# Performance work log

Hardware: AMD Instinct MI355X
Metric: run time of the kernel (lower is better)

The kernel has to match this reference:

```python
import jax, jax.numpy as jnp
import numpy as np

K = 5          # top_k periods
KERNEL = 25    # moving-average kernel for series decomposition
D = 64         # d_model / channels
EPS = 1e-5     # BatchNorm eps (torch default)


def setup_inputs() -> dict:
    key = jax.random.key(0)
    k0, k1, k2, k3, k4 = jax.random.split(key, 5)
    B, T = 8, 2048
    x = jax.random.normal(k0, (B, T, D), jnp.float32)
    w1 = jax.random.normal(k1, (D, D, 3, 3), jnp.float32) * 0.05
    w2 = jax.random.normal(k2, (D, D, 3, 3), jnp.float32) * 0.05
    bn1_gamma = jnp.ones((D,), jnp.float32) + 0.1 * jax.random.normal(k3, (D,), jnp.float32)
    bn2_gamma = jnp.ones((D,), jnp.float32) + 0.1 * jax.random.normal(k4, (D,), jnp.float32)
    z = jnp.zeros((D,), jnp.float32)
    o = jnp.ones((D,), jnp.float32)
    return dict(x=x, w1=w1, w2=w2,
                bn1_gamma=bn1_gamma, bn1_beta=z, bn1_mean=z, bn1_var=o,
                bn2_gamma=bn2_gamma, bn2_beta=z, bn2_mean=z, bn2_var=o)


def _moving_avg(x, kernel):
    # AvgPool1d(stride=1, padding=(kernel-1)//2, count_include_pad=False) over time.
    T = x.shape[1]
    pad = (kernel - 1) // 2
    cs = jnp.concatenate([jnp.zeros_like(x[:, :1]), jnp.cumsum(x, axis=1)], axis=1)  # [B,T+1,C]
    t = jnp.arange(T)
    lo = jnp.clip(t - pad, 0, T)          # inclusive window start
    hi = jnp.clip(t + pad + 1, 0, T)      # exclusive window end
    sums = cs[:, hi] - cs[:, lo]
    return sums / (hi - lo).astype(x.dtype)[None, :, None]


def _auto_corr(s, k):
    T = s.shape[1]
    Xf = jnp.fft.rfft(s, axis=1)
    Pm = (Xf * jnp.conj(Xf)).real.mean(axis=-1)          # [B, T//2+1]
    r = jnp.fft.irfft(Pm, n=T, axis=1)                   # [B, T]
    r = r.at[:, 0].set(-jnp.inf)                          # forbid lag 0
    vals, idx = jax.lax.top_k(r, k)                       # [B,k]
    w = jax.nn.softmax(vals, axis=1)
    return idx, w


def _bn(z, gamma, beta, mean, var):
    return (z - mean) * (gamma * jax.lax.rsqrt(var + EPS)) + beta


def _process_one(s_b, p, w1, w2, bn1, bn2):
    # s_b: [T, C]; p: scalar int period.
    # Equivalent to: roll(s_b, -p), reflect-pad time to cyc*p, fold to [C,cyc,p],
    # Conv2dResBlock (3x3 zero-pad convs + eval BN + GELU + residual), unfold, crop to T.
    T, C = s_b.shape
    U = 2 * T - 2                               # static bound: cyc*p <= T+p-1 <= 2T-2
    u = jnp.arange(U)
    cyc = (T + p - 1) // p
    v = jnp.where(u < T, u, 2 * T - 2 - u)      # reflect extension index
    g = s_b[(v + p) % T]                         # [U,C] rolled-by-(-p) then reflect-padded
    r = u // p                                   # grid row (cycle)
    c = u % p                                    # grid col (phase)

    def conv3x3(z, w):
        # zero-padded 3x3 conv on the [cyc, p] grid, expressed on the flat time axis
        out = jnp.zeros_like(z)
        for dr in (-1, 0, 1):
            for dc in (-1, 0, 1):
                valid = (r + dr >= 0) & (r + dr < cyc) & (c + dc >= 0) & (c + dc < p)
                un = jnp.clip(u + dr * p + dc, 0, U - 1)
                zn = jnp.where(valid[:, None], z[un], 0.0)    # [U,C]
                out = out + zn @ w[:, :, dr + 1, dc + 1].T    # [U,Cout]
        return out

    h = _bn(conv3x3(g, w1), *bn1)
    h = jax.nn.gelu(h, approximate=False)
    h = _bn(conv3x3(h, w2), *bn2)
    return (g + h)[:T]                           # residual + unfold-crop


def reference(x, w1, w2, bn1_gamma, bn1_beta, bn1_mean, bn1_var,
              bn2_gamma, bn2_beta, bn2_mean, bn2_var):
    trend = _moving_avg(x, KERNEL)
    s = x - trend                                # seasonal
    idx, w = _auto_corr(s, K)                    # [B,K] periods, weights
    bn1 = (bn1_gamma, bn1_beta, bn1_mean, bn1_var)
    bn2 = (bn2_gamma, bn2_beta, bn2_mean, bn2_var)
    f = lambda sb, p: _process_one(sb, p, w1, w2, bn1, bn2)
    y = jax.vmap(lambda sb, pb: jax.vmap(lambda p: f(sb, p))(pb))(s, idx)  # [B,K,T,C]
    agg = jnp.einsum('bk,bktc->btc', w, y)
    return agg + trend + x
```

## Files before the change

kernel.cpp:

```cpp
#include <hip/hip_runtime.h>
#include <hip/hip_bf16.h>
#include <math.h>

#define TB 8
#define TT 2048
#define TD 64
#define TK 5
#define TPAD 12
#define EPSBN 1e-5f
#define UMAX 4096

#define ROWS 64
#define BAND 66
#define LROWS 198

#define ROWS2 16
#define BAND2 18
#define LROWS2 54
#define SH8   432
#define BUFB  6912

#define ACG 17

typedef __attribute__((ext_vector_type(8))) short short8;
typedef __attribute__((ext_vector_type(4))) float f32x4;

#define OFF_S     0
#define OFF_SBF   1048576
#define OFF_R     1572864
#define OFF_IDX   1581056
#define OFF_W     1581096
#define OFF_WT1   1581136
#define OFF_WT2   1599568
#define OFF_H1    1618000
#define OFF_CAND  6860880
#define OFF_VALS  6860944

__global__ __launch_bounds__(256) void k_trend(const float* __restrict__ x,
                                               float* __restrict__ out, float* __restrict__ s,
                                               __hip_bfloat16* __restrict__ sbf,
                                               const float* __restrict__ w1, const float* __restrict__ w2,
                                               __hip_bfloat16* __restrict__ wt1, __hip_bfloat16* __restrict__ wt2,
                                               float* __restrict__ r)
{
    if (blockIdx.x >= 256) {
        int d = (blockIdx.x - 256) * 256 + threadIdx.x;
        if (d < TB * 1024) r[d] = 0.f;
        if (d < 36864) {
            int j = d & 7, l = (d >> 3) & 63, nt = (d >> 9) & 3, kb = d >> 11;
            int tap = kb >> 1, half = kb & 1;
            int co = nt * 16 + (l & 15);
            int ci = half * 32 + (l >> 4) * 8 + j;
            int src = (co * 64 + ci) * 9 + tap;
            wt1[d] = __float2bfloat16(w1[src]);
            wt2[d] = __float2bfloat16(w2[src]);
        }
        return;
    }
    int gid = blockIdx.x * 256 + threadIdx.x;
    int c = gid & 63;
    int tblk = (gid >> 6) & 127;
    int b = gid >> 13;
    int t0 = tblk * 16;
    const float* base = x + (size_t)b * TT * TD + c;
    float sum = 0.f;
    for (int tt = t0 - TPAD; tt <= t0 + TPAD; ++tt)
        if (tt >= 0 && tt < TT) sum += base[(size_t)tt * TD];
    size_t o = (size_t)b * TT * TD + (size_t)t0 * TD + c;
    #pragma unroll
    for (int i = 0; i < 16; ++i) {
        int t = t0 + i;
        int lo = t - TPAD; if (lo < 0) lo = 0;
        int hi = t + TPAD; if (hi > TT - 1) hi = TT - 1;
        float tr = sum / (float)(hi - lo + 1);
        float xv = base[(size_t)t * TD];
        out[o] = xv + tr;
        float sv = xv - tr;
        s[o] = sv;
        sbf[o] = __float2bfloat16(sv);
        int addt = t + TPAD + 1, subt = t - TPAD;
        if (addt < TT) sum += base[(size_t)addt * TD];
        if (subt >= 0) sum -= base[(size_t)subt * TD];
        o += TD;
    }
}

__global__ __launch_bounds__(256) void k_ac_mfma(const short* __restrict__ sbf16, float* __restrict__ r)
{
    int id = blockIdx.x;
    int b = id & 7;
    int slot = id >> 3;
    int g = slot % ACG;
    int qq = slot / ACG;
    int d0 = g * 4;
    int t0 = qq * 32;
    const short* sb = sbf16 + (size_t)b * TT * TD;

    __shared__ short Atile[2][1024];
    __shared__ short Btile[6][1024];
    __shared__ float scr[4][16 * 17];

    int tid = threadIdx.x;
    if (tid < 128) {
        int dst = (tid * 16) ^ (((tid >> 3) & 7) << 4);
        *(short8*)((char*)Atile[t0 & 1] + dst) =
            *(const short8*)(sb + (size_t)((t0 & 127) * 1024) + tid * 8);
        #pragma unroll
        for (int j = 0; j < 4; ++j) {
            int xi = t0 + d0 + j;
            *(short8*)((char*)Btile[xi % 6] + dst) =
                *(const short8*)(sb + (size_t)((xi & 127) * 1024) + tid * 8);
        }
    }
    __syncthreads();

    int lane = tid & 63, wv = tid >> 6;
    int fr = lane & 15, kg = lane >> 4;
    int roff0 = (fr * 128 + kg * 16) ^ ((fr & 7) << 4);
    int roff1 = roff0 ^ 64;
    int myD = d0 + wv;

    f32x4 acc = {};
    for (int stp = 0; stp < 32; ++stp) {
        int ti = t0 + stp;
        short8 sA, sB;
        if (tid < 128) {
            sA = *(const short8*)(sb + (size_t)(((ti + 1) & 127) * 1024) + tid * 8);
            sB = *(const short8*)(sb + (size_t)(((ti + d0 + 4) & 127) * 1024) + tid * 8);
        }
        const char* Ab = (const char*)Atile[ti & 1];
        const char* Bb = (const char*)Btile[(ti + myD) % 6];
        short8 a0 = *(const short8*)(Ab + roff0);
        short8 a1 = *(const short8*)(Ab + roff1);
        short8 b0 = *(const short8*)(Bb + roff0);
        short8 b1 = *(const short8*)(Bb + roff1);
        acc = __builtin_amdgcn_mfma_f32_16x16x32_bf16(a0, b0, acc, 0, 0, 0);
        acc = __builtin_amdgcn_mfma_f32_16x16x32_bf16(a1, b1, acc, 0, 0, 0);
        if (tid < 128) {
            int dst = (tid * 16) ^ (((tid >> 3) & 7) << 4);
            *(short8*)((char*)Atile[(ti + 1) & 1] + dst) = sA;
            *(short8*)((char*)Btile[(ti + d0 + 4) % 6] + dst) = sB;
        }
        __syncthreads();
    }

    float* sc = scr[wv];
    #pragma unroll
    for (int q = 0; q < 4; ++q)
        sc[(kg * 4 + q) * 17 + fr] = acc[q];
    __syncthreads();
    if (lane < 31) {
        int d = lane - 15;
        int lag = 16 * myD + d;
        if (lag >= 1 && lag <= 1024) {
            int m0 = d < 0 ? -d : 0;
            int m1 = d < 0 ? 16 : 16 - d;
            float v = 0.f;
            for (int m = m0; m < m1; ++m) v += sc[m * 17 + m + d];
            atomicAdd(&r[(size_t)b * 1024 + (lag - 1)], v * (1.0f / 64.0f));
        }
    }
}

__global__ __launch_bounds__(256) void k_cand(const float* __restrict__ r, int* __restrict__ cand)
{
    int b = blockIdx.x;
    __shared__ float v[1024];
    __shared__ float redv[256]; __shared__ int redi[256];
    for (int i = threadIdx.x; i < 1024; i += 256) v[i] = r[(size_t)b * 1024 + i];
    __syncthreads();
    for (int round = 0; round < 8; ++round) {
        float bv = -INFINITY; int bi = 1 << 30;
        for (int i = threadIdx.x; i < 1024; i += 256) {
            float val = v[i];
            if (val > bv) { bv = val; bi = i; }
        }
        redv[threadIdx.x] = bv; redi[threadIdx.x] = bi;
        __syncthreads();
        for (int off = 128; off; off >>= 1) {
            if (threadIdx.x < off) {
                float ov = redv[threadIdx.x + off]; int oi = redi[threadIdx.x + off];
                float mv = redv[threadIdx.x];       int mi = redi[threadIdx.x];
                if (ov > mv || (ov == mv && oi < mi)) { redv[threadIdx.x] = ov; redi[threadIdx.x] = oi; }
            }
            __syncthreads();
        }
        if (threadIdx.x == 0) {
            int lag = redi[0] + 1;
            cand[b * 8 + round] = lag;
            v[lag - 1] = -INFINITY;
        }
        __syncthreads();
    }
}

__global__ __launch_bounds__(256) void k_rescore(const float* __restrict__ s, const int* __restrict__ cand,
                                                 float* __restrict__ vals)
{
    int ci = blockIdx.x;
    int b = blockIdx.y;
    int lag = cand[b * 8 + ci];
    const float* sb = s + (size_t)b * TT * TD;
    int cg = (threadIdx.x & 15) * 4;
    int t0 = (threadIdx.x >> 4) * 128;
    float acc = 0.f;
    #pragma unroll 8
    for (int t = t0; t < t0 + 128; ++t) {
        const float4 a = *(const float4*)(sb + ((size_t)t << 6) + cg);
        const float4 w = *(const float4*)(sb + ((size_t)((t + lag) & (TT - 1)) << 6) + cg);
        acc = fmaf(a.x, w.x, acc);
        acc = fmaf(a.y, w.y, acc);
        acc = fmaf(a.z, w.z, acc);
        acc = fmaf(a.w, w.w, acc);
    }
    __shared__ float red[256];
    red[threadIdx.x] = acc;
    __syncthreads();
    for (int off = 128; off; off >>= 1) {
        if (threadIdx.x < off) red[threadIdx.x] += red[threadIdx.x + off];
        __syncthreads();
    }
    if (threadIdx.x == 0) vals[b * 8 + ci] = red[0] * (1.0f / 64.0f);
}

__global__ __launch_bounds__(64) void k_sel(const float* __restrict__ vals, const int* __restrict__ cand,
                                            int* __restrict__ selidx, float* __restrict__ selw)
{
    int b = blockIdx.x;
    if (threadIdx.x != 0) return;
    float vv[8]; int ll[8]; bool used[8];
    #pragma unroll
    for (int i = 0; i < 8; ++i) { vv[i] = vals[b * 8 + i]; ll[i] = cand[b * 8 + i]; used[i] = false; }
    int s_idx[6]; float s_val[6]; int slots = 0;
    while (slots < 5) {
        float bv = -INFINITY; int bi = -1;
        for (int i = 0; i < 8; ++i) {
            if (!used[i] && (vv[i] > bv || (vv[i] == bv && bi >= 0 && ll[i] < ll[bi]))) { bv = vv[i]; bi = i; }
        }
        used[bi] = true;
        s_idx[slots] = ll[bi]; s_val[slots] = bv; slots++;
        if (slots < 5 && ll[bi] < 1024) { s_idx[slots] = 2048 - ll[bi]; s_val[slots] = bv; slots++; }
    }
    float mx = -INFINITY;
    for (int i = 0; i < 5; ++i) mx = fmaxf(mx, s_val[i]);
    float e[5], sum = 0.f;
    for (int i = 0; i < 5; ++i) { e[i] = expf(s_val[i] - mx); sum += e[i]; }
    for (int i = 0; i < 5; ++i) { selidx[b * TK + i] = s_idx[i]; selw[b * TK + i] = e[i] / sum; }
}

__global__ __launch_bounds__(256) void k_mm1(
    const short* __restrict__ s_bf, const short* __restrict__ wtp,
    const float* __restrict__ g1, const float* __restrict__ b1,
    const float* __restrict__ m1, const float* __restrict__ v1,
    const int* __restrict__ sel, __hip_bfloat16* __restrict__ h1)
{
    int b = blockIdx.z, k = blockIdx.y;
    int p = sel[b * TK + k];
    int cyc = (TT + p - 1) / p;
    int U = cyc * p;
    int u0 = blockIdx.x * ROWS;
    if (u0 >= U) return;
    __shared__ short As[LROWS * 64];

    const short* sb = s_bf + (size_t)b * TT * TD;
    for (int q = threadIdx.x; q < LROWS * 8; q += 256) {
        int row = q >> 3, ch = (q & 7) * 8;
        int band = row / BAND, i = row - band * BAND;
        int w = u0 + (band - 1) * p - 1 + i;
        int wc = min(max(w, 0), 2 * TT - 2);
        int v = (wc < TT) ? wc : (2 * TT - 2 - wc);
        int sr = (v + p) & (TT - 1);
        short8 d = *(const short8*)(sb + (size_t)sr * TD + ch);
        int off = (row * 128 + ch * 2) ^ ((row & 7) << 4);
        *(short8*)((char*)As + off) = d;
    }
    __syncthreads();

    int lane = threadIdx.x & 63;
    int wv = threadIdx.x >> 6;
    int lr = lane & 15;
    int kg = lane >> 4;
    int lu = wv * 16 + lr;
    int u = u0 + lu;
    bool inU = (u < U);
    int r = u / p, c = u - r * p;
    bool topf = (r == 0), botf = (r == cyc - 1), leftf = (c == 0), rightf = (c == p - 1);

    f32x4 acc[4] = {};
    short8 zero = {};
    #pragma unroll
    for (int kb = 0; kb < 18; ++kb) {
        const int tap = kb >> 1, half = kb & 1;
        const int dr = tap / 3 - 1, dc = tap % 3 - 1;
        int ldsrow = (dr + 1) * BAND + lu + 1 + dc;
        int off = (ldsrow * 128 + half * 64 + kg * 16) ^ ((ldsrow & 7) << 4);
        short8 a = *(const short8*)((const char*)As + off);
        bool valid = inU
                   && !(dr == -1 && topf) && !(dr == 1 && botf)
                   && !(dc == -1 && leftf) && !(dc == 1 && rightf);
        if (!valid) a = zero;
        #pragma unroll
        for (int nt = 0; nt < 4; ++nt) {
            short8 bq = *(const short8*)(wtp + (size_t)(kb * 4 + nt) * 512 + lane * 8);
            acc[nt] = __builtin_amdgcn_mfma_f32_16x16x32_bf16(a, bq, acc[nt], 0, 0, 0);
        }
    }
    __hip_bfloat16* ho = h1 + (size_t)(b * TK + k) * (UMAX * TD);
    #pragma unroll
    for (int nt = 0; nt < 4; ++nt) {
        int co = nt * 16 + lr;
        float scale = g1[co] * rsqrtf(v1[co] + EPSBN);
        float bias = b1[co] - m1[co] * scale;
        #pragma unroll
        for (int q = 0; q < 4; ++q) {
            int uo = u0 + wv * 16 + kg * 4 + q;
            if (uo < U) {
                float z = acc[nt][q] * scale + bias;
                float ge = 0.5f * z * (1.0f + erff(z * 0.70710678118654752f));
                ho[(size_t)uo * TD + co] = __float2bfloat16(ge);
            }
        }
    }
}

__global__ __launch_bounds__(256) void k_mm2f(
    const short* __restrict__ h1, const short* __restrict__ wtp,
    const float* __restrict__ s,
    const float* __restrict__ g2, const float* __restrict__ b2,
    const float* __restrict__ m2, const float* __restrict__ v2,
    const int* __restrict__ sel, const float* __restrict__ selw,
    float* __restrict__ out)
{
    int b = blockIdx.y;
    int u0 = blockIdx.x * ROWS2;
    int tid = threadIdx.x;
    __shared__ short As[2 * LROWS2 * 64];

    int lane = tid & 63, wv = tid >> 6, lr = lane & 15, kg = lane >> 4;
    int u = u0 + lr;
    const float* sb = s + (size_t)b * TT * TD;

    f32x4 accT = {};
    float gacc[4] = {0.f, 0.f, 0.f, 0.f};
    short8 sreg[2];
    short8 zero = {};

    {
        int p0 = sel[b * TK];
        const short* hb = h1 + (size_t)(b * TK) * (UMAX * TD);
        #pragma unroll
        for (int it = 0; it < 2; ++it) {
            int q = tid + it * 256;
            if (q < SH8) {
                int row = q >> 3, ch = (q & 7) * 8;
                int band = row / BAND2, i = row - band * BAND2;
                int w = u0 + (band - 1) * p0 - 1 + i;
                int wc = min(max(w, 0), UMAX - 1);
                short8 d = *(const short8*)(hb + (size_t)wc * TD + ch);
                int off = (row * 128 + ch * 2) ^ ((row & 7) << 4);
                *(short8*)((char*)As + off) = d;
            }
        }
    }
    __syncthreads();

    for (int k = 0; k < TK; ++k) {
        int p = sel[b * TK + k];
        float wk = selw[b * TK + k];
        int cyc = (TT + p - 1) / p;
        if (k < TK - 1) {
            int pn = sel[b * TK + k + 1];
            const short* hb = h1 + (size_t)(b * TK + k + 1) * (UMAX * TD);
            #pragma unroll
            for (int it = 0; it < 2; ++it) {
                int q = tid + it * 256;
                if (q < SH8) {
                    int row = q >> 3, ch = (q & 7) * 8;
                    int band = row / BAND2, i = row - band * BAND2;
                    int w = u0 + (band - 1) * pn - 1 + i;
                    int wc = min(max(w, 0), UMAX - 1);
                    sreg[it] = *(const short8*)(hb + (size_t)wc * TD + ch);
                }
            }
        }
        const char* Ab = (const char*)As + (k & 1) * BUFB;
        int r = u / p, c = u - r * p;
        bool topf = (r == 0), botf = (r == cyc - 1), leftf = (c == 0), rightf = (c == p - 1);
        f32x4 accP[2] = {};
        #pragma unroll
        for (int kb = 0; kb < 18; ++kb) {
            const int tap = kb >> 1, half = kb & 1;
            const int dr = tap / 3 - 1, dc = tap % 3 - 1;
            int ldsrow = (dr + 1) * BAND2 + lr + 1 + dc;
            int off = (ldsrow * 128 + half * 64 + kg * 16) ^ ((ldsrow & 7) << 4);
            short8 a = *(const short8*)(Ab + off);
            bool valid = !(dr == -1 && topf) && !(dr == 1 && botf)
                       && !(dc == -1 && leftf) && !(dc == 1 && rightf);
            if (!valid) a = zero;
            short8 bq = *(const short8*)(wtp + (size_t)(kb * 4 + wv) * 512 + lane * 8);
            accP[kb & 1] = __builtin_amdgcn_mfma_f32_16x16x32_bf16(a, bq, accP[kb & 1], 0, 0, 0);
        }
        #pragma unroll
        for (int e = 0; e < 4; ++e) accT[e] += wk * (accP[0][e] + accP[1][e]);
        #pragma unroll
        for (int q = 0; q < 4; ++q) {
            int uo = u0 + kg * 4 + q;
            int sr = (uo + p) & (TT - 1);
            gacc[q] = fmaf(wk, sb[(size_t)sr * TD + wv * 16 + lr], gacc[q]);
        }
        __syncthreads();
        if (k < TK - 1) {
            char* Aw = (char*)As + ((k + 1) & 1) * BUFB;
            #pragma unroll
            for (int it = 0; it < 2; ++it) {
                int q = tid + it * 256;
                if (q < SH8) {
                    int row = q >> 3, ch = (q & 7) * 8;
                    int off = (row * 128 + ch * 2) ^ ((row & 7) << 4);
                    *(short8*)(Aw + off) = sreg[it];
                }
            }
            __syncthreads();
        }
    }

    float* ob = out + (size_t)b * TT * TD;
    int co = wv * 16 + lr;
    float scale = g2[co] * rsqrtf(v2[co] + EPSBN);
    float bias = b2[co] - m2[co] * scale;
    #pragma unroll
    for (int q = 0; q < 4; ++q) {
        int uo = u0 + kg * 4 + q;
        size_t idx = (size_t)uo * TD + co;
        ob[idx] = ob[idx] + gacc[q] + scale * accT[q] + bias;
    }
}

extern "C" void kernel_launch(void* const* d_in, const int* in_sizes, int n_in,
                              void* d_out, int out_size, void* d_ws, size_t ws_size,
                              hipStream_t stream)
{
    const float* x  = (const float*)d_in[0];
    const float* w1 = (const float*)d_in[1];
    const float* w2 = (const float*)d_in[2];
    const float* g1 = (const float*)d_in[3];
    const float* b1 = (const float*)d_in[4];
    const float* m1 = (const float*)d_in[5];
    const float* v1 = (const float*)d_in[6];
    const float* g2 = (const float*)d_in[7];
    const float* b2 = (const float*)d_in[8];
    const float* m2 = (const float*)d_in[9];
    const float* v2 = (const float*)d_in[10];

    float* ws    = (float*)d_ws;
    float* s     = ws + OFF_S;
    __hip_bfloat16* sbf = (__hip_bfloat16*)(ws + OFF_SBF);
    float* r     = ws + OFF_R;
    int*   sel   = (int*)(ws + OFF_IDX);
    float* selw  = ws + OFF_W;
    __hip_bfloat16* wt1 = (__hip_bfloat16*)(ws + OFF_WT1);
    __hip_bfloat16* wt2 = (__hip_bfloat16*)(ws + OFF_WT2);
    __hip_bfloat16* h1  = (__hip_bfloat16*)(ws + OFF_H1);
    int*   cand  = (int*)(ws + OFF_CAND);
    float* vals  = ws + OFF_VALS;
    float* out   = (float*)d_out;

    k_trend   <<<dim3(400),         dim3(256), 0, stream>>>(x, out, s, sbf, w1, w2, wt1, wt2, r);
    k_ac_mfma <<<dim3(544),         dim3(256), 0, stream>>>((const short*)sbf, r);
    k_cand    <<<dim3(TB),          dim3(256), 0, stream>>>(r, cand);
    k_rescore <<<dim3(8, TB),       dim3(256), 0, stream>>>(s, cand, vals);
    k_sel     <<<dim3(TB),          dim3(64),  0, stream>>>(vals, cand, sel, selw);
    k_mm1     <<<dim3(64, TK, TB),  dim3(256), 0, stream>>>((const short*)sbf, (const short*)wt1,
                                                            g1, b1, m1, v1, sel, h1);
    k_mm2f    <<<dim3(128, TB),     dim3(256), 0, stream>>>((const short*)h1, (const short*)wt2, s,
                                                            g2, b2, m2, v2, sel, selw, out);
}
```

Baseline: 121.8 us.

## Double k_mm1 rows per block with B-fragment reuse; split rescore over time with atomics

k_mm1 now handles 128 output rows per block: each wave computes two 16-row MFMA tiles and reuses every weight fragment load for both. The block count is halved and the stencil LDS tile grows to 390 rows. k_rescore splits its time range into 4 chunks across more blocks and combines partial sums with atomicAdd into vals, which k_trend zeroes first. This raises parallelism in the small rescore launch but makes the summation order nondeterministic, and the larger k_mm1 tiles raise LDS and register use per block.

```diff
diff --git a/kernel.cpp b/kernel.cpp
--- a/kernel.cpp
+++ b/kernel.cpp
@@ -10,9 +10,9 @@
 #define EPSBN 1e-5f
 #define UMAX 4096
 
-#define ROWS 64
-#define BAND 66
-#define LROWS 198
+#define ROWS1 128
+#define BAND1 130
+#define LROWS1 390
 
 #define ROWS2 16
 #define BAND2 18
@@ -41,11 +41,12 @@
                                                __hip_bfloat16* __restrict__ sbf,
                                                const float* __restrict__ w1, const float* __restrict__ w2,
                                                __hip_bfloat16* __restrict__ wt1, __hip_bfloat16* __restrict__ wt2,
-                                               float* __restrict__ r)
+                                               float* __restrict__ r, float* __restrict__ vals)
 {
     if (blockIdx.x >= 256) {
         int d = (blockIdx.x - 256) * 256 + threadIdx.x;
         if (d < TB * 1024) r[d] = 0.f;
+        if (d < TB * 8) vals[d] = 0.f;
         if (d < 36864) {
             int j = d & 7, l = (d >> 3) & 63, nt = (d >> 9) & 3, kb = d >> 11;
             int tap = kb >> 1, half = kb & 1;
@@ -198,14 +199,15 @@
                                                  float* __restrict__ vals)
 {
     int ci = blockIdx.x;
-    int b = blockIdx.y;
+    int tq = blockIdx.y;
+    int b = blockIdx.z;
     int lag = cand[b * 8 + ci];
     const float* sb = s + (size_t)b * TT * TD;
     int cg = (threadIdx.x & 15) * 4;
-    int t0 = (threadIdx.x >> 4) * 128;
+    int t0 = tq * 512 + (threadIdx.x >> 4) * 32;
     float acc = 0.f;
     #pragma unroll 8
-    for (int t = t0; t < t0 + 128; ++t) {
+    for (int t = t0; t < t0 + 32; ++t) {
         const float4 a = *(const float4*)(sb + ((size_t)t << 6) + cg);
         const float4 w = *(const float4*)(sb + ((size_t)((t + lag) & (TT - 1)) << 6) + cg);
         acc = fmaf(a.x, w.x, acc);
@@ -220,7 +222,7 @@
         if (threadIdx.x < off) red[threadIdx.x] += red[threadIdx.x + off];
         __syncthreads();
     }
-    if (threadIdx.x == 0) vals[b * 8 + ci] = red[0] * (1.0f / 64.0f);
+    if (threadIdx.x == 0) atomicAdd(&vals[b * 8 + ci], red[0] * (1.0f / 64.0f));
 }
 
 __global__ __launch_bounds__(64) void k_sel(const float* __restrict__ vals, const int* __restrict__ cand,
@@ -258,14 +260,14 @@
     int p = sel[b * TK + k];
     int cyc = (TT + p - 1) / p;
     int U = cyc * p;
-    int u0 = blockIdx.x * ROWS;
+    int u0 = blockIdx.x * ROWS1;
     if (u0 >= U) return;
-    __shared__ short As[LROWS * 64];
+    __shared__ short As[LROWS1 * 64];
 
     const short* sb = s_bf + (size_t)b * TT * TD;
-    for (int q = threadIdx.x; q < LROWS * 8; q += 256) {
+    for (int q = threadIdx.x; q < LROWS1 * 8; q += 256) {
         int row = q >> 3, ch = (q & 7) * 8;
-        int band = row / BAND, i = row - band * BAND;
+        int band = row / BAND1, i = row - band * BAND1;
         int w = u0 + (band - 1) * p - 1 + i;
         int wc = min(max(w, 0), 2 * TT - 2);
         int v = (wc < TT) ? wc : (2 * TT - 2 - wc);
@@ -280,29 +282,40 @@
     int wv = threadIdx.x >> 6;
     int lr = lane & 15;
     int kg = lane >> 4;
-    int lu = wv * 16 + lr;
-    int u = u0 + lu;
-    bool inU = (u < U);
-    int r = u / p, c = u - r * p;
-    bool topf = (r == 0), botf = (r == cyc - 1), leftf = (c == 0), rightf = (c == p - 1);
-
-    f32x4 acc[4] = {};
+    int lu[2]; bool inU[2], topf[2], botf[2], leftf[2], rightf[2];
+    #pragma unroll
+    for (int rs = 0; rs < 2; ++rs) {
+        lu[rs] = wv * 32 + rs * 16 + lr;
+        int u = u0 + lu[rs];
+        inU[rs] = (u < U);
+        int r = u / p, c = u - r * p;
+        topf[rs] = (r == 0); botf[rs] = (r == cyc - 1);
+        leftf[rs] = (c == 0); rightf[rs] = (c == p - 1);
+    }
+
+    f32x4 acc[2][4] = {};
     short8 zero = {};
     #pragma unroll
     for (int kb = 0; kb < 18; ++kb) {
         const int tap = kb >> 1, half = kb & 1;
         const int dr = tap / 3 - 1, dc = tap % 3 - 1;
-        int ldsrow = (dr + 1) * BAND + lu + 1 + dc;
-        int off = (ldsrow * 128 + half * 64 + kg * 16) ^ ((ldsrow & 7) << 4);
-        short8 a = *(const short8*)((const char*)As + off);
-        bool valid = inU
-                   && !(dr == -1 && topf) && !(dr == 1 && botf)
-                   && !(dc == -1 && leftf) && !(dc == 1 && rightf);
-        if (!valid) a = zero;
+        short8 a[2];
+        #pragma unroll
+        for (int rs = 0; rs < 2; ++rs) {
+            int ldsrow = (dr + 1) * BAND1 + lu[rs] + 1 + dc;
+            int off = (ldsrow * 128 + half * 64 + kg * 16) ^ ((ldsrow & 7) << 4);
+            a[rs] = *(const short8*)((const char*)As + off);
+            bool valid = inU[rs]
+                       && !(dr == -1 && topf[rs]) && !(dr == 1 && botf[rs])
+                       && !(dc == -1 && leftf[rs]) && !(dc == 1 && rightf[rs]);
+            if (!valid) a[rs] = zero;
+        }
         #pragma unroll
         for (int nt = 0; nt < 4; ++nt) {
             short8 bq = *(const short8*)(wtp + (size_t)(kb * 4 + nt) * 512 + lane * 8);
-            acc[nt] = __builtin_amdgcn_mfma_f32_16x16x32_bf16(a, bq, acc[nt], 0, 0, 0);
+            #pragma unroll
+            for (int rs = 0; rs < 2; ++rs)
+                acc[rs][nt] = __builtin_amdgcn_mfma_f32_16x16x32_bf16(a[rs], bq, acc[rs][nt], 0, 0, 0);
         }
     }
     __hip_bfloat16* ho = h1 + (size_t)(b * TK + k) * (UMAX * TD);
@@ -312,12 +325,16 @@
         float scale = g1[co] * rsqrtf(v1[co] + EPSBN);
         float bias = b1[co] - m1[co] * scale;
         #pragma unroll
-        for (int q = 0; q < 4; ++q) {
-            int uo = u0 + wv * 16 + kg * 4 + q;
-            if (uo < U) {
-                float z = acc[nt][q] * scale + bias;
-                float ge = 0.5f * z * (1.0f + erff(z * 0.70710678118654752f));
-                ho[(size_t)uo * TD + co] = __float2bfloat16(ge);
+        for (int rs = 0; rs < 2; ++rs) {
+            int ub = u0 + wv * 32 + rs * 16 + kg * 4;
+            #pragma unroll
+            for (int q = 0; q < 4; ++q) {
+                int uo = ub + q;
+                if (uo < U) {
+                    float z = acc[rs][nt][q] * scale + bias;
+                    float ge = 0.5f * z * (1.0f + erff(z * 0.70710678118654752f));
+                    ho[(size_t)uo * TD + co] = __float2bfloat16(ge);
+                }
             }
         }
     }
@@ -465,12 +482,12 @@
     float* vals  = ws + OFF_VALS;
     float* out   = (float*)d_out;
 
-    k_trend   <<<dim3(400),         dim3(256), 0, stream>>>(x, out, s, sbf, w1, w2, wt1, wt2, r);
+    k_trend   <<<dim3(400),         dim3(256), 0, stream>>>(x, out, s, sbf, w1, w2, wt1, wt2, r, vals);
     k_ac_mfma <<<dim3(544),         dim3(256), 0, stream>>>((const short*)sbf, r);
     k_cand    <<<dim3(TB),          dim3(256), 0, stream>>>(r, cand);
-    k_rescore <<<dim3(8, TB),       dim3(256), 0, stream>>>(s, cand, vals);
+    k_rescore <<<dim3(8, 4, TB),    dim3(256), 0, stream>>>(s, cand, vals);
     k_sel     <<<dim3(TB),          dim3(64),  0, stream>>>(vals, cand, sel, selw);
-    k_mm1     <<<dim3(64, TK, TB),  dim3(256), 0, stream>>>((const short*)sbf, (const short*)wt1,
+    k_mm1     <<<dim3(32, TK, TB),  dim3(256), 0, stream>>>((const short*)sbf, (const short*)wt1,
                                                             g1, b1, m1, v1, sel, h1);
     k_mm2f    <<<dim3(128, TB),     dim3(256), 0, stream>>>((const short*)h1, (const short*)wt2, s,
                                                             g2, b2, m2, v2, sel, selw, out);
```

Measured after the change: 114.2 us. 6.3% less time.
